# Kernel tuning notes

Hardware: AMD Instinct MI355X
Metric: run time of the kernel (lower is better)

The kernel has to match this reference:

```python
import jax, jax.numpy as jnp
import numpy as np

C = 64      # planes_num = prod(discrete_shape)
H = 256     # cont_size[0]
W = 256     # cont_size[1]
L0 = 1024   # len(grid[0])
L1 = 1024   # len(grid[1])
A = -0.75   # bicubic convolution constant (matches PyTorch grid_sample)


def _cubic_weights(t):
    # t: fractional part in [0,1), shape (N,). Weights for taps at offsets -1,0,1,2.
    t2 = t * t
    t3 = t2 * t
    w0 = A * (t3 - 2.0 * t2 + t)                 # cubic_conv2(1+t)
    w1 = (A + 2.0) * t3 - (A + 3.0) * t2 + 1.0   # cubic_conv1(t)
    s = 1.0 - t
    s2 = s * s
    w2 = (A + 2.0) * s2 * s - (A + 3.0) * s2 + 1.0  # cubic_conv1(1-t)
    u = 1.0 + s                                   # = 2 - t
    w3 = A * (u * u * u) - 5.0 * A * (u * u) + 8.0 * A * u - 4.0 * A  # cubic_conv2(2-t)
    return jnp.stack([w0, w1, w2, w3], axis=-1)   # (N,4)


def _prep(g, size):
    # align_corners=True unnormalization: [-1,1] -> [0, size-1]
    x = (g + 1.0) * 0.5 * (size - 1)
    x0 = jnp.floor(x)
    t = x - x0
    idx = x0.astype(jnp.int32)[:, None] + jnp.arange(-1, 3)  # (N,4) tap indices
    idx = jnp.clip(idx, 0, size - 1)                          # padding_mode='border'
    return idx, _cubic_weights(t)


def setup_inputs() -> dict:
    key = jax.random.key(0)
    k1, k2, k3 = jax.random.split(key, 3)
    values = jax.random.uniform(k1, (1, C, H, W), dtype=jnp.float32)  # torch.rand init
    g0 = jax.random.uniform(k2, (L0,), dtype=jnp.float32) * 2.0 - 1.0  # normalized coords
    g1 = jax.random.uniform(k3, (L1,), dtype=jnp.float32) * 2.0 - 1.0
    return {"values": values, "g0": g0, "g1": g1}


def reference(values, g0, g1):
    # preprocess_grid: meshgrid(grid[::-1], 'ij') stacked -> grid[i,j] = (x=g1[i], y=g0[j])
    # grid_sample(values, grid, bicubic, border, align_corners=True)
    v = values[0]                 # (C,H,W)
    xi, wx = _prep(g1, W)         # x taps/weights, (L1,4)
    yi, wy = _prep(g0, H)         # y taps/weights, (L0,4)
    out = jnp.zeros((v.shape[0], g1.shape[0], g0.shape[0]), values.dtype)  # (C,L1,L0)
    for a in range(4):            # 4x4 separable bicubic taps (fixed small loop)
        xa = xi[:, a][:, None]    # (L1,1)
        wa = wx[:, a][:, None]    # (L1,1)
        for b in range(4):
            w = wa * wy[:, b][None, :]                 # (L1,L0)
            out = out + w * v[:, yi[:, b][None, :], xa]  # gather -> (C,L1,L0)
    return out[None]              # (1, C, L1, L0)
```

## Files before the change

kernel.cpp:

```cpp
#include <hip/hip_runtime.h>

#define C_   64
#define H_   256
#define W_   256
#define L0_  1024
#define L1_  1024
#define JT   32
#define ROWP 33
#define HYR  259

__device__ __forceinline__ void cubic_weights(float t, float w[4]) {
    const float A = -0.75f;
    float t2 = t * t, t3 = t2 * t;
    w[0] = A * (t3 - 2.0f * t2 + t);
    w[1] = (A + 2.0f) * t3 - (A + 3.0f) * t2 + 1.0f;
    float s = 1.0f - t, s2 = s * s;
    w[2] = (A + 2.0f) * s2 * s - (A + 3.0f) * s2 + 1.0f;
    float u = 2.0f - t, u2 = u * u;
    w[3] = A * u2 * u - 5.0f * A * u2 + 8.0f * A * u - 4.0f * A;
}

__global__ __launch_bounds__(256, 3) void bicubic_pad(const float* __restrict__ v,
                                                      const float* __restrict__ g0,
                                                      const float* __restrict__ g1,
                                                      float* __restrict__ out) {
    __shared__ float  hy[HYR * ROWP];
    __shared__ float4 xw[L1_];

    const int t  = threadIdx.x;
    const int c  = blockIdx.y;
    const int j0 = blockIdx.x * JT;

    {
        const int ib = t * 4;
#pragma unroll
        for (int s = 0; s < 4; ++s) {
            int i = ib + s;
            float x  = (g1[i] + 1.0f) * 0.5f * (float)(W_ - 1);
            float x0 = floorf(x);
            int   ix = min(max((int)x0, 0), W_ - 1);
            float w4[4]; cubic_weights(x - x0, w4);
            unsigned b3 = (__float_as_uint(w4[3]) & 0xFFFFFF00u) | (unsigned)ix;
            xw[i] = make_float4(w4[0], w4[1], w4[2], __uint_as_float(b3));
        }
    }

    const int lane = t & 63;
    const int wv   = t >> 6;

    {
        const int x1 = lane;
        const float* vc = v + (size_t)c * (H_ * W_);
#pragma unroll
        for (int jj = 0; jj < JT / 4; ++jj) {
            int j = wv * (JT / 4) + jj;
            float xg = (g0[j0 + j] + 1.0f) * 0.5f * (float)(H_ - 1);
            float x0 = floorf(xg);
            int   iy = (int)x0;
            float wy[4]; cubic_weights(xg - x0, wy);
            const float* r0 = vc + min(max(iy - 1, 0), H_ - 1) * W_;
            const float* r1 = vc + min(max(iy,     0), H_ - 1) * W_;
            const float* r2 = vc + min(max(iy + 1, 0), H_ - 1) * W_;
            const float* r3 = vc + min(max(iy + 2, 0), H_ - 1) * W_;
#pragma unroll
            for (int k = 0; k < 4; ++k) {
                int x_ = x1 + 64 * k;
                float val = wy[0] * r0[x_] + wy[1] * r1[x_]
                          + wy[2] * r2[x_] + wy[3] * r3[x_];
                hy[(x_ + 1) * ROWP + j] = val;
                if (x_ == 0)   hy[j] = val;
                if (x_ == 255) {
                    hy[257 * ROWP + j] = val;
                    hy[258 * ROWP + j] = val;
                }
            }
        }
    }
    __syncthreads();

    {
        const int jl    = t & 31;
        const int ihalf = (t >> 5) & 1;
        int i = wv * 256 + ihalf;
        float* op = out + (size_t)c * ((size_t)L1_ * L0_)
                  + (size_t)i * L0_ + j0 + jl;
#pragma unroll 4
        for (int it = 0; it < 128; ++it, i += 2, op += 2 * L0_) {
            float4 w = xw[i];
            int xk0 = (int)(__float_as_uint(w.w) & 0xFFu);
            const float* hp = &hy[xk0 * ROWP + jl];
            float o = w.x * hp[0]
                    + w.y * hp[ROWP]
                    + w.z * hp[2 * ROWP]
                    + w.w * hp[3 * ROWP];
            *op = o;
        }
    }
}

extern "C" void kernel_launch(void* const* d_in, const int* in_sizes, int n_in,
                              void* d_out, int out_size, void* d_ws, size_t ws_size,
                              hipStream_t stream) {
    const float* values = (const float*)d_in[0];
    const float* g0     = (const float*)d_in[1];
    const float* g1     = (const float*)d_in[2];
    float* out          = (float*)d_out;

    dim3 grid(L0_ / JT, C_);
    bicubic_pad<<<grid, 256, 0, stream>>>(values, g0, g1, out);
}
```

Baseline: 72.30 us.

## Process two channels per block with paired float2 intermediate tile

Each block now handles two channels, so the x-weight table setup and per-column y-weight computation are amortized over twice the output. The vertical intermediate is stored as float2 pairs, and the fourth x-weight is derived from the partition of unity, which removes one shared-memory weight load. Shared memory per block roughly doubles and occupancy drops to 2 blocks per CU. The kernel remains bound by output writes, so the gain depends on how much the setup overhead mattered.

```diff
diff --git a/kernel.cpp b/kernel.cpp
--- a/kernel.cpp
+++ b/kernel.cpp
@@ -20,15 +20,16 @@
     w[3] = A * u2 * u - 5.0f * A * u2 + 8.0f * A * u - 4.0f * A;
 }
 
-__global__ __launch_bounds__(256, 3) void bicubic_pad(const float* __restrict__ v,
-                                                      const float* __restrict__ g0,
-                                                      const float* __restrict__ g1,
-                                                      float* __restrict__ out) {
-    __shared__ float  hy[HYR * ROWP];
-    __shared__ float4 xw[L1_];
+__global__ __launch_bounds__(256, 2) void bicubic_pair(const float* __restrict__ v,
+                                                       const float* __restrict__ g0,
+                                                       const float* __restrict__ g1,
+                                                       float* __restrict__ out) {
+    __shared__ float2 hy2[HYR * ROWP];
+    __shared__ float2 wAB[L1_];
+    __shared__ float  wC [L1_];
 
     const int t  = threadIdx.x;
-    const int c  = blockIdx.y;
+    const int c0 = blockIdx.y * 2;
     const int j0 = blockIdx.x * JT;
 
     {
@@ -40,8 +41,9 @@
             float x0 = floorf(x);
             int   ix = min(max((int)x0, 0), W_ - 1);
             float w4[4]; cubic_weights(x - x0, w4);
-            unsigned b3 = (__float_as_uint(w4[3]) & 0xFFFFFF00u) | (unsigned)ix;
-            xw[i] = make_float4(w4[0], w4[1], w4[2], __uint_as_float(b3));
+            wAB[i] = make_float2(w4[0], w4[1]);
+            wC[i]  = __uint_as_float((__float_as_uint(w4[2]) & 0xFFFFFF00u)
+                                     | (unsigned)ix);
         }
     }
 
@@ -49,8 +51,8 @@
     const int wv   = t >> 6;
 
     {
-        const int x1 = lane;
-        const float* vc = v + (size_t)c * (H_ * W_);
+        const float* vA = v + (size_t)c0 * (H_ * W_);
+        const float* vB = vA + (H_ * W_);
 #pragma unroll
         for (int jj = 0; jj < JT / 4; ++jj) {
             int j = wv * (JT / 4) + jj;
@@ -58,20 +60,23 @@
             float x0 = floorf(xg);
             int   iy = (int)x0;
             float wy[4]; cubic_weights(xg - x0, wy);
-            const float* r0 = vc + min(max(iy - 1, 0), H_ - 1) * W_;
-            const float* r1 = vc + min(max(iy,     0), H_ - 1) * W_;
-            const float* r2 = vc + min(max(iy + 1, 0), H_ - 1) * W_;
-            const float* r3 = vc + min(max(iy + 2, 0), H_ - 1) * W_;
+            const int y0 = min(max(iy - 1, 0), H_ - 1) * W_;
+            const int y1 = min(max(iy,     0), H_ - 1) * W_;
+            const int y2 = min(max(iy + 1, 0), H_ - 1) * W_;
+            const int y3 = min(max(iy + 2, 0), H_ - 1) * W_;
 #pragma unroll
             for (int k = 0; k < 4; ++k) {
-                int x_ = x1 + 64 * k;
-                float val = wy[0] * r0[x_] + wy[1] * r1[x_]
-                          + wy[2] * r2[x_] + wy[3] * r3[x_];
-                hy[(x_ + 1) * ROWP + j] = val;
-                if (x_ == 0)   hy[j] = val;
+                int x_ = lane + 64 * k;
+                float a = wy[0] * vA[y0 + x_] + wy[1] * vA[y1 + x_]
+                        + wy[2] * vA[y2 + x_] + wy[3] * vA[y3 + x_];
+                float b = wy[0] * vB[y0 + x_] + wy[1] * vB[y1 + x_]
+                        + wy[2] * vB[y2 + x_] + wy[3] * vB[y3 + x_];
+                float2 val = make_float2(a, b);
+                hy2[(x_ + 1) * ROWP + j] = val;
+                if (x_ == 0)   hy2[j] = val;
                 if (x_ == 255) {
-                    hy[257 * ROWP + j] = val;
-                    hy[258 * ROWP + j] = val;
+                    hy2[257 * ROWP + j] = val;
+                    hy2[258 * ROWP + j] = val;
                 }
             }
         }
@@ -82,18 +87,22 @@
         const int jl    = t & 31;
         const int ihalf = (t >> 5) & 1;
         int i = wv * 256 + ihalf;
-        float* op = out + (size_t)c * ((size_t)L1_ * L0_)
+        float* o0 = out + (size_t)c0 * ((size_t)L1_ * L0_)
                   + (size_t)i * L0_ + j0 + jl;
+        float* o1 = o0 + (size_t)L1_ * L0_;
 #pragma unroll 4
-        for (int it = 0; it < 128; ++it, i += 2, op += 2 * L0_) {
-            float4 w = xw[i];
-            int xk0 = (int)(__float_as_uint(w.w) & 0xFFu);
-            const float* hp = &hy[xk0 * ROWP + jl];
-            float o = w.x * hp[0]
-                    + w.y * hp[ROWP]
-                    + w.z * hp[2 * ROWP]
-                    + w.w * hp[3 * ROWP];
-            *op = o;
+        for (int it = 0; it < 128; ++it, i += 2, o0 += 2 * L0_, o1 += 2 * L0_) {
+            float2 ab = wAB[i];
+            float  cw = wC[i];
+            int    ix = (int)(__float_as_uint(cw) & 0xFFu);
+            float  w3 = 1.0f - ab.x - ab.y - cw;
+            const float2* hp = &hy2[ix * ROWP + jl];
+            float2 h0 = hp[0];
+            float2 h1 = hp[ROWP];
+            float2 h2 = hp[2 * ROWP];
+            float2 h3 = hp[3 * ROWP];
+            *o0 = ab.x * h0.x + ab.y * h1.x + cw * h2.x + w3 * h3.x;
+            *o1 = ab.x * h0.y + ab.y * h1.y + cw * h2.y + w3 * h3.y;
         }
     }
 }
@@ -106,6 +115,6 @@
     const float* g1     = (const float*)d_in[2];
     float* out          = (float*)d_out;
 
-    dim3 grid(L0_ / JT, C_);
-    bicubic_pad<<<grid, 256, 0, stream>>>(values, g0, g1, out);
+    dim3 grid(L0_ / JT, C_ / 2);
+    bicubic_pair<<<grid, 256, 0, stream>>>(values, g0, g1, out);
 }
```

Measured after the change: 70.46 us. 2.5% less time.
